# Kernel optimization log

Hardware: AMD Instinct MI355X
Metric: run time of the kernel (lower is better)

## Reference

```python
import jax, jax.numpy as jnp
import numpy as np

POOL = 7
IMG_H, IMG_W = 1024, 1024
EPS = 1e-3  # keras BatchNormalization default epsilon


def crop_and_resize(fmap, boxes, ph, pw):
    # TF tf.image.crop_and_resize (bilinear), box_indices == batch index of each roi.
    # fmap: [B,H,W,C], boxes: [B,N,4] normalized (y1,x1,y2,x2) -> [B,N,ph,pw,C]
    B, H, W, C = fmap.shape
    y1, x1, y2, x2 = jnp.split(boxes, 4, axis=-1)  # each [B,N,1]
    fy = jnp.arange(ph, dtype=boxes.dtype) / (ph - 1)
    fx = jnp.arange(pw, dtype=boxes.dtype) / (pw - 1)
    ys = (y1 + (y2 - y1) * fy) * (H - 1)  # [B,N,ph]
    xs = (x1 + (x2 - x1) * fx) * (W - 1)  # [B,N,pw]
    y0 = jnp.floor(ys)
    x0 = jnp.floor(xs)
    wy = (ys - y0)[:, :, :, None, None]  # [B,N,ph,1,1]
    wx = (xs - x0)[:, :, None, :, None]  # [B,N,1,pw,1]
    y0i = jnp.clip(y0.astype(jnp.int32), 0, H - 1)
    y1i = jnp.clip(y0i + 1, 0, H - 1)
    x0i = jnp.clip(x0.astype(jnp.int32), 0, W - 1)
    x1i = jnp.clip(x0i + 1, 0, W - 1)
    b = jnp.arange(B)[:, None, None, None]
    yi0 = y0i[:, :, :, None]; yi1 = y1i[:, :, :, None]   # [B,N,ph,1]
    xi0 = x0i[:, :, None, :]; xi1 = x1i[:, :, None, :]   # [B,N,1,pw]
    v00 = fmap[b, yi0, xi0]  # [B,N,ph,pw,C]
    v01 = fmap[b, yi0, xi1]
    v10 = fmap[b, yi1, xi0]
    v11 = fmap[b, yi1, xi1]
    top = v00 + (v01 - v00) * wx
    bot = v10 + (v11 - v10) * wx
    return top + (bot - top) * wy


def pyramid_roi_align(rois, fmaps, pool):
    # rois are stop-gradient in the original layer
    rois = jax.lax.stop_gradient(rois)
    y1, x1, y2, x2 = jnp.split(rois, 4, axis=-1)
    h = y2 - y1
    w = x2 - x1
    scale = 256.0 / np.sqrt(float(IMG_H * IMG_W))
    lvl = jnp.log2(jnp.maximum(jnp.sqrt(h * w), 1e-9) / scale)
    lvl = jnp.clip(4 + jnp.round(lvl).astype(jnp.int32), 2, 5)[..., 0]  # [B,N]
    B, N = rois.shape[:2]
    C = fmaps[0].shape[-1]
    out = jnp.zeros((B, N, pool, pool, C), fmaps[0].dtype)
    for i, fm in enumerate(fmaps):  # levels 2..5, fixed small loop
        sel = (lvl == i + 2)[:, :, None, None, None]
        out = jnp.where(sel, crop_and_resize(fm, rois, pool, pool), out)
    return out


def bn_train(x, gamma, beta):
    # keras BatchNorm with training=True: biased batch stats over all axes but channel
    m = x.mean(axis=(0, 1))
    v = x.var(axis=(0, 1))
    return (x - m) * jax.lax.rsqrt(v + EPS) * gamma + beta


def setup_inputs() -> dict:
    key = jax.random.key(0)
    ks = jax.random.split(key, 12)
    B, N, C, F = 2, 1000, 256, 1024
    # rois: valid boxes, sizes spanning all pyramid levels
    tl = jax.random.uniform(ks[0], (B, N, 2), jnp.float32, 0.0, 0.6)
    sz = jax.random.uniform(ks[1], (B, N, 2), jnp.float32, 0.02, 0.4)
    br = jnp.minimum(tl + sz, 1.0)
    rois = jnp.concatenate([tl[..., :1], tl[..., 1:], br[..., :1], br[..., 1:]], axis=-1)
    s = 0.02
    return {
        "rois": rois,
        "p2": jax.random.normal(ks[2], (B, 256, 256, C), jnp.float32),
        "p3": jax.random.normal(ks[3], (B, 128, 128, C), jnp.float32),
        "p4": jax.random.normal(ks[4], (B, 64, 64, C), jnp.float32),
        "p5": jax.random.normal(ks[5], (B, 32, 32, C), jnp.float32),
        "conv1_w": jax.random.normal(ks[6], (POOL, POOL, C, F), jnp.float32) * s,
        "conv1_b": jnp.zeros((F,), jnp.float32),
        "bn1_g": jnp.ones((F,), jnp.float32),
        "bn1_b": jnp.zeros((F,), jnp.float32),
        "conv2_w": jax.random.normal(ks[7], (F, F), jnp.float32) * s,
        "conv2_b": jnp.zeros((F,), jnp.float32),
        "bn2_g": jnp.ones((F,), jnp.float32),
        "bn2_b": jnp.zeros((F,), jnp.float32),
        "cls_w": jax.random.normal(ks[8], (F, 2), jnp.float32) * s,
        "cls_b": jnp.zeros((2,), jnp.float32),
        "delta_w": jax.random.normal(ks[9], (F, 8), jnp.float32) * s,
        "delta_b": jnp.zeros((8,), jnp.float32),
    }


def reference(rois, p2, p3, p4, p5, conv1_w, conv1_b, bn1_g, bn1_b,
              conv2_w, conv2_b, bn2_g, bn2_b, cls_w, cls_b, delta_w, delta_b):
    B, N = rois.shape[:2]
    n_classes = cls_w.shape[-1]
    pooled = pyramid_roi_align(rois, (p2, p3, p4, p5), POOL)  # [B,N,7,7,C]
    # Conv2D(F,(7,7),'valid') on a 7x7 input == full contraction over (h,w,c)
    x = jnp.einsum('bnhwc,hwcf->bnf', pooled, conv1_w) + conv1_b
    x = jax.nn.relu(bn_train(x, bn1_g, bn1_b))
    x = x @ conv2_w + conv2_b  # 1x1 conv == dense
    shared = jax.nn.relu(bn_train(x, bn2_g, bn2_b))  # [B,N,F]
    logits = shared @ cls_w + cls_b                  # [B,N,n_classes]
    probs = jax.nn.softmax(logits, axis=-1)
    deltas = (shared @ delta_w + delta_b).reshape(B, N, n_classes, 4)
    return logits, probs, deltas
```

## Files before the change

### kernel.cpp

```cpp
#include <hip/hip_runtime.h>
#include <hip/hip_bf16.h>

#define NB     2
#define NROI   1000
#define CIN    256
#define FDIM   1024
#define M_ROWS 2000
#define K1     12544
#define EPSBN  1e-3f
#define MN     (M_ROWS * FDIM)

typedef short bf16x8 __attribute__((ext_vector_type(8)));
typedef short bf16x4 __attribute__((ext_vector_type(4)));
typedef float f32x4  __attribute__((ext_vector_type(4)));

__device__ __forceinline__ void gld_lds16(const void* g, void* l) {
  __builtin_amdgcn_global_load_lds((const __attribute__((address_space(1))) char*)g,
                                   (__attribute__((address_space(3))) char*)l, 16, 0, 0);
}

__global__ __launch_bounds__(256) void prep_kernel(
    const float* __restrict__ rois,
    const float* __restrict__ p2, const float* __restrict__ p3,
    const float* __restrict__ p4, const float* __restrict__ p5,
    __hip_bfloat16* __restrict__ pooled,
    const float* __restrict__ conv1_w, __hip_bfloat16* __restrict__ w1t,
    const float* __restrict__ conv2_w, __hip_bfloat16* __restrict__ w2t,
    float* __restrict__ stats) {
  __shared__ float tt[64][65];
  int idx = blockIdx.x;
  int t = threadIdx.x;

  if (idx == 0) {
#pragma unroll
    for (int i = 0; i < 4; i++)
      ((f32x4*)stats)[t + i * 256] = f32x4{0, 0, 0, 0};
    return;
  }

  if (idx < 1 + M_ROWS) {
    int rn = idx - 1;
    int b = rn / NROI;

    const float* roi = rois + (size_t)rn * 4;
    float y1 = roi[0], x1 = roi[1], y2 = roi[2], x2 = roi[3];
    float h = y2 - y1, w = x2 - x1;
    float lvl = log2f(fmaxf(sqrtf(h * w), 1e-9f) * 4.0f);
    int li = 4 + (int)rintf(lvl);
    li = min(max(li, 2), 5) - 2;

    const float* fm; int H;
    switch (li) {
      case 0:  fm = p2; H = 256; break;
      case 1:  fm = p3; H = 128; break;
      case 2:  fm = p4; H = 64;  break;
      default: fm = p5; H = 32;  break;
    }
    int W = H;
    const float* fb = fm + (size_t)b * H * W * CIN;

    int lane = t & 63, wv = t >> 6;
    int c4 = lane * 4;

    for (int pos = wv; pos < 49; pos += 4) {
      int py = pos / 7, px = pos - py * 7;
      float fy = (float)py / 6.0f, fx = (float)px / 6.0f;
      float ys = (y1 + (y2 - y1) * fy) * (float)(H - 1);
      float xs = (x1 + (x2 - x1) * fx) * (float)(W - 1);
      float y0f = floorf(ys), x0f = floorf(xs);
      float wy = ys - y0f, wx = xs - x0f;
      int y0 = min(max((int)y0f, 0), H - 1);
      int x0 = min(max((int)x0f, 0), W - 1);
      int y1i = min(y0 + 1, H - 1);
      int x1i = min(x0 + 1, W - 1);

      f32x4 v00 = *(const f32x4*)(fb + ((size_t)y0 * W + x0) * CIN + c4);
      f32x4 v01 = *(const f32x4*)(fb + ((size_t)y0 * W + x1i) * CIN + c4);
      f32x4 v10 = *(const f32x4*)(fb + ((size_t)y1i * W + x0) * CIN + c4);
      f32x4 v11 = *(const f32x4*)(fb + ((size_t)y1i * W + x1i) * CIN + c4);

      f32x4 top = v00 + (v01 - v00) * wx;
      f32x4 bot = v10 + (v11 - v10) * wx;
      f32x4 val = top + (bot - top) * wy;

      bf16x4 o;
#pragma unroll
      for (int j = 0; j < 4; j++) {
        __hip_bfloat16 hh = __float2bfloat16(val[j]);
        o[j] = *reinterpret_cast<short*>(&hh);
      }
      *(bf16x4*)((short*)pooled + ((size_t)rn * 49 + pos) * CIN + c4) = o;
    }
    return;
  }

  const float* W; short* WT; int K, N, bx, by;
  if (idx < 1 + M_ROWS + 3136) {
    int wk = idx - (1 + M_ROWS);
    W = conv1_w; WT = (short*)w1t; K = K1; N = FDIM;
    bx = wk % 196; by = wk / 196;
  } else {
    int wk = idx - (1 + M_ROWS + 3136);
    W = conv2_w; WT = (short*)w2t; K = FDIM; N = FDIM;
    bx = wk % 16; by = wk / 16;
  }
  int k0 = bx * 64, n0 = by * 64;
  int r = t >> 2, c = t & 3;
#pragma unroll
  for (int i = 0; i < 4; i++) {
    int cg = c * 4 + i;
    f32x4 v = *(const f32x4*)(W + (size_t)(k0 + r) * N + n0 + cg * 4);
#pragma unroll
    for (int j = 0; j < 4; j++) tt[cg * 4 + j][r] = v[j];
  }
  __syncthreads();
  int n = t >> 2, g = t & 3;
#pragma unroll
  for (int i = 0; i < 2; i++) {
    int seg = g * 2 + i;
    bf16x8 o;
#pragma unroll
    for (int j = 0; j < 8; j++) {
      __hip_bfloat16 hh = __float2bfloat16(tt[n][seg * 8 + j]);
      o[j] = *reinterpret_cast<short*>(&hh);
    }
    *(bf16x8*)(WT + (size_t)(n0 + n) * K + k0 + seg * 8) = o;
  }
}

template<int KSLICES>
__global__ __launch_bounds__(512) void gemm8w(const short* __restrict__ A,
                                              const short* __restrict__ BT,
                                              float* __restrict__ P,
                                              int M, int N, int K) {
  __shared__ short As[4 * 128 * 32];
  __shared__ short Bs[4 * 256 * 32];

  int nwg = gridDim.x;
  int bid = blockIdx.x;
  int cpx = nwg >> 3;
  int wg = (bid & 7) * cpx + (bid >> 3);

  int MT = (M + 127) >> 7;
  int NTn = N >> 8;
  int tiles = MT * NTn;
  int ks = wg / tiles;
  int rem = wg % tiles;
  int tm = rem % MT, tn = rem / MT;
  int m0 = tm * 128, n0 = tn * 256;
  int Kc = K / KSLICES;
  int NT = Kc >> 6;
  size_t kb = (size_t)ks * Kc;

  int tid = threadIdx.x;
  int lane = tid & 63, wid = tid >> 6;
  int wr = wid >> 2, wc = wid & 3;

  int srow = tid >> 2;
  int g = (tid & 3) ^ (srow & 3);
  const short* Agb  = A  + (size_t)min(m0 + srow, M - 1) * K + kb + g * 8;
  const short* Bgb0 = BT + (size_t)(n0 + srow) * K + kb + g * 8;
  const short* Bgb1 = Bgb0 + (size_t)128 * K;
  int aoff  = wid * 512;
  int boff0 = wid * 512;
  int boff1 = 4096 + wid * 512;

  int lr = lane & 15;
  int slotoff = ((lane >> 4) ^ (lane & 3)) * 8;
  const short* Ard = As + (wr * 64 + lr) * 32 + slotoff;
  const short* Brd = Bs + (wc * 64 + lr) * 32 + slotoff;

  f32x4 acc[4][4] = {};

#define STAGE(s) do {                                                        \
    int ts_ = (s) >> 1, kh_ = (s) & 1, b_ = ts_ & 1;                         \
    int ko_ = ts_ * 64 + kh_ * 32;                                           \
    short* Ad_ = (short*)As + (b_ * 2 + kh_) * 4096 + aoff;                  \
    short* Bd_ = (short*)Bs + (b_ * 2 + kh_) * 8192;                         \
    gld_lds16(Agb + ko_, Ad_);                                               \
    gld_lds16(Bgb0 + ko_, Bd_ + boff0);                                      \
    gld_lds16(Bgb1 + ko_, Bd_ + boff1);                                      \
  } while (0)

  STAGE(0); STAGE(1); STAGE(2);

  for (int t = 0; t < NT; ++t) {
    int b = t & 1;
#pragma unroll
    for (int kh = 0; kh < 2; ++kh) {
      __builtin_amdgcn_sched_barrier(0);
      if (t < NT - 1)      asm volatile("s_waitcnt vmcnt(6)" ::: "memory");
      else if (kh == 0)    asm volatile("s_waitcnt vmcnt(3)" ::: "memory");
      else                 asm volatile("s_waitcnt vmcnt(0)" ::: "memory");
      __builtin_amdgcn_s_barrier();
      __builtin_amdgcn_sched_barrier(0);

      const short* Ab = Ard + (b * 2 + kh) * 4096;
      const short* Bb = Brd + (b * 2 + kh) * 8192;
      bf16x8 af[4], bf_[4];
#pragma unroll
      for (int mi = 0; mi < 4; mi++) af[mi] = *(const bf16x8*)(Ab + mi * 512);
#pragma unroll
      for (int ni = 0; ni < 4; ni++) bf_[ni] = *(const bf16x8*)(Bb + ni * 512);

      if (kh == 0) { if (t + 1 < NT) STAGE(2 * t + 3); }
      else         { if (t + 2 < NT) STAGE(2 * t + 4); }

      __builtin_amdgcn_sched_barrier(0);
      asm volatile("s_waitcnt lgkmcnt(0)" ::: "memory");
      __builtin_amdgcn_sched_barrier(0);
      __builtin_amdgcn_s_setprio(1);
#pragma unroll
      for (int mi = 0; mi < 4; mi++)
#pragma unroll
        for (int ni = 0; ni < 4; ni++)
          acc[mi][ni] = __builtin_amdgcn_mfma_f32_16x16x32_bf16(af[mi], bf_[ni], acc[mi][ni], 0, 0, 0);
      __builtin_amdgcn_s_setprio(0);
    }
  }
#undef STAGE

  float* Pb = P + (size_t)ks * M * N;
  int crow = (lane >> 4) * 4, ccol = lane & 15;
#pragma unroll
  for (int mi = 0; mi < 4; mi++) {
    int rb = m0 + wr * 64 + mi * 16 + crow;
#pragma unroll
    for (int ni = 0; ni < 4; ni++) {
      int col = n0 + wc * 64 + ni * 16 + ccol;
#pragma unroll
      for (int r = 0; r < 4; r++) {
        int row = rb + r;
        if (row < M) Pb[(size_t)row * N + col] = acc[mi][ni][r];
      }
    }
  }
}

__global__ void reduce_bias_stats(const float* __restrict__ P, const float* __restrict__ bias,
                                  float* __restrict__ X, float* __restrict__ stats,
                                  int M, int KS) {
  int t = threadIdx.x;
  int col = t * 4;
  f32x4 bv = *(const f32x4*)(bias + col);
  f32x4 s = {0, 0, 0, 0}, q = {0, 0, 0, 0};
  for (int r = blockIdx.x; r < M; r += gridDim.x) {
    size_t base = (size_t)r * FDIM + col;
    f32x4 v = *(const f32x4*)(P + base);
    for (int c = 1; c < KS; c++)
      v = v + *(const f32x4*)(P + (size_t)c * MN + base);
    v = v + bv;
    *(f32x4*)(X + base) = v;
    s = s + v;
    q = q + v * v;
  }
#pragma unroll
  for (int j = 0; j < 4; j++) {
    atomicAdd(&stats[col + j], s[j]);
    atomicAdd(&stats[FDIM + col + j], q[j]);
  }
}

__global__ void bn_norm_relu_bf16(const float* __restrict__ X, const float* __restrict__ stats,
                                  const float* __restrict__ g, const float* __restrict__ bta,
                                  __hip_bfloat16* __restrict__ obf, int M) {
  int idx = blockIdx.x * blockDim.x + threadIdx.x;
  if (idx >= M * FDIM) return;
  int f = idx & (FDIM - 1);
  float inv_m = 1.0f / (float)M;
  float mean = stats[f] * inv_m;
  float var = stats[FDIM + f] * inv_m - mean * mean;
  float xn = (X[idx] - mean) * rsqrtf(var + EPSBN) * g[f] + bta[f];
  obf[idx] = __float2bfloat16(fmaxf(xn, 0.0f));
}

__global__ void heads_bn(const float* __restrict__ X2, const float* __restrict__ stats,
                         const float* __restrict__ gg, const float* __restrict__ bb,
                         const float* __restrict__ cls_w, const float* __restrict__ cls_b,
                         const float* __restrict__ dw, const float* __restrict__ db,
                         float* __restrict__ out) {
  int row = blockIdx.x * 4 + (threadIdx.x >> 6);
  int lane = threadIdx.x & 63;
  if (row >= M_ROWS) return;
  const float* xrow = X2 + (size_t)row * FDIM;
  float inv_m = 1.0f / (float)M_ROWS;
  float a[10];
#pragma unroll
  for (int j = 0; j < 10; j++) a[j] = 0.0f;
  for (int k = lane; k < FDIM; k += 64) {
    float mean = stats[k] * inv_m;
    float var = stats[FDIM + k] * inv_m - mean * mean;
    float v = fmaxf((xrow[k] - mean) * rsqrtf(var + EPSBN) * gg[k] + bb[k], 0.0f);
    a[0] += v * cls_w[k * 2 + 0];
    a[1] += v * cls_w[k * 2 + 1];
#pragma unroll
    for (int j = 0; j < 8; j++) a[2 + j] += v * dw[k * 8 + j];
  }
#pragma unroll
  for (int j = 0; j < 10; j++)
    for (int o = 32; o > 0; o >>= 1) a[j] += __shfl_xor(a[j], o, 64);
  if (lane == 0) {
    float l0 = a[0] + cls_b[0], l1 = a[1] + cls_b[1];
    out[row * 2 + 0] = l0;
    out[row * 2 + 1] = l1;
    float mx = fmaxf(l0, l1);
    float e0 = expf(l0 - mx), e1 = expf(l1 - mx);
    float inv = 1.0f / (e0 + e1);
    out[4000 + row * 2 + 0] = e0 * inv;
    out[4000 + row * 2 + 1] = e1 * inv;
#pragma unroll
    for (int j = 0; j < 8; j++) out[8000 + row * 8 + j] = a[2 + j] + db[j];
  }
}

extern "C" void kernel_launch(void* const* d_in, const int* in_sizes, int n_in,
                              void* d_out, int out_size, void* d_ws, size_t ws_size,
                              hipStream_t stream) {
  const float* rois    = (const float*)d_in[0];
  const float* p2      = (const float*)d_in[1];
  const float* p3      = (const float*)d_in[2];
  const float* p4      = (const float*)d_in[3];
  const float* p5      = (const float*)d_in[4];
  const float* conv1_w = (const float*)d_in[5];
  const float* conv1_b = (const float*)d_in[6];
  const float* bn1_g   = (const float*)d_in[7];
  const float* bn1_b   = (const float*)d_in[8];
  const float* conv2_w = (const float*)d_in[9];
  const float* conv2_b = (const float*)d_in[10];
  const float* bn2_g   = (const float*)d_in[11];
  const float* bn2_b   = (const float*)d_in[12];
  const float* cls_w   = (const float*)d_in[13];
  const float* cls_b   = (const float*)d_in[14];
  const float* delta_w = (const float*)d_in[15];
  const float* delta_b = (const float*)d_in[16];
  float* out = (float*)d_out;

  char* ws = (char*)d_ws;
  size_t off = 0;
  __hip_bfloat16* pooled = (__hip_bfloat16*)(ws + off); off += (size_t)M_ROWS * K1 * 2;
  __hip_bfloat16* w1t    = (__hip_bfloat16*)(ws + off); off += (size_t)K1 * FDIM * 2;
  __hip_bfloat16* w2t    = (__hip_bfloat16*)(ws + off); off += (size_t)FDIM * FDIM * 2;
  float* stats1          = (float*)(ws + off);          off += 2 * FDIM * 4;
  float* stats2          = (float*)(ws + off);          off += 2 * FDIM * 4;
  char*  Preg            = ws + off;                    off += (size_t)4 * MN * 4;
  float* part1        = (float*)Preg;
  float* x1           = (float*)Preg;
  __hip_bfloat16* x1n = (__hip_bfloat16*)pooled;
  float* part2        = (float*)Preg;
  float* x2           = (float*)Preg;

  prep_kernel<<<1 + M_ROWS + 3136 + 256, 256, 0, stream>>>(
      rois, p2, p3, p4, p5, pooled, conv1_w, w1t, conv2_w, w2t, stats1);

  gemm8w<4><<<256, 512, 0, stream>>>((const short*)pooled, (const short*)w1t, part1,
                                     M_ROWS, FDIM, K1);
  reduce_bias_stats<<<256, 256, 0, stream>>>(part1, conv1_b, x1, stats1, M_ROWS, 4);

  bn_norm_relu_bf16<<<MN / 256, 256, 0, stream>>>(x1, stats1, bn1_g, bn1_b, x1n, M_ROWS);

  gemm8w<4><<<256, 512, 0, stream>>>((const short*)x1n, (const short*)w2t, part2,
                                     M_ROWS, FDIM, FDIM);
  reduce_bias_stats<<<256, 256, 0, stream>>>(part2, conv2_b, x2, stats2, M_ROWS, 4);

  heads_bn<<<(M_ROWS + 3) / 4, 256, 0, stream>>>(x2, stats2, bn2_g, bn2_b,
                                                 cls_w, cls_b, delta_w, delta_b, out);

  (void)in_sizes; (void)n_in; (void)out_size; (void)ws_size;
}
```

Measured before the change: 210.8 us.

## Deepen GEMM LDS pipeline to six stages, split ROI pooling, restructure heads kernel

The GEMM main loop moves from a double-buffered 2x32 scheme to a six-slot ring of 32-wide K stages with five loads in flight, and K becomes a compile-time template parameter so the loop can be unrolled. The aim is to hide global-to-LDS latency more deeply. ROI pooling now uses two blocks per ROI to give the prep kernel more parallelism. The heads kernel precomputes BN scale/shift and transposed head weights in shared memory and processes 16 rows per block. The deeper ring raises LDS use per block, which may reduce occupancy.

```diff
diff --git a/kernel.cpp b/kernel.cpp
--- a/kernel.cpp
+++ b/kernel.cpp
@@ -18,6 +18,8 @@
   __builtin_amdgcn_global_load_lds((const __attribute__((address_space(1))) char*)g,
                                    (__attribute__((address_space(3))) char*)l, 16, 0, 0);
 }
+
+#define VWAIT(n) asm volatile("s_waitcnt vmcnt(" #n ")" ::: "memory")
 
 __global__ __launch_bounds__(256) void prep_kernel(
     const float* __restrict__ rois,
@@ -38,8 +40,9 @@
     return;
   }
 
-  if (idx < 1 + M_ROWS) {
-    int rn = idx - 1;
+  if (idx < 1 + 2 * M_ROWS) {
+    int rr = idx - 1;
+    int rn = rr >> 1, half = rr & 1;
     int b = rn / NROI;
 
     const float* roi = rois + (size_t)rn * 4;
@@ -62,7 +65,7 @@
     int lane = t & 63, wv = t >> 6;
     int c4 = lane * 4;
 
-    for (int pos = wv; pos < 49; pos += 4) {
+    for (int pos = half * 4 + wv; pos < 49; pos += 8) {
       int py = pos / 7, px = pos - py * 7;
       float fy = (float)py / 6.0f, fx = (float)px / 6.0f;
       float ys = (y1 + (y2 - y1) * fy) * (float)(H - 1);
@@ -95,12 +98,12 @@
   }
 
   const float* W; short* WT; int K, N, bx, by;
-  if (idx < 1 + M_ROWS + 3136) {
-    int wk = idx - (1 + M_ROWS);
+  if (idx < 1 + 2 * M_ROWS + 3136) {
+    int wk = idx - (1 + 2 * M_ROWS);
     W = conv1_w; WT = (short*)w1t; K = K1; N = FDIM;
     bx = wk % 196; by = wk / 196;
   } else {
-    int wk = idx - (1 + M_ROWS + 3136);
+    int wk = idx - (1 + 2 * M_ROWS + 3136);
     W = conv2_w; WT = (short*)w2t; K = FDIM; N = FDIM;
     bx = wk % 16; by = wk / 16;
   }
@@ -128,13 +131,18 @@
   }
 }
 
-template<int KSLICES>
+template<int KSLICES, int KTOT>
 __global__ __launch_bounds__(512) void gemm8w(const short* __restrict__ A,
                                               const short* __restrict__ BT,
                                               float* __restrict__ P,
-                                              int M, int N, int K) {
-  __shared__ short As[4 * 128 * 32];
-  __shared__ short Bs[4 * 256 * 32];
+                                              int M, int N) {
+  constexpr int Kc = KTOT / KSLICES;
+  constexpr int S2 = Kc / 32;
+  static_assert(Kc % 64 == 0 && S2 >= 8, "K slice shape");
+  constexpr int K = KTOT;
+
+  __shared__ short As[6 * 4096];
+  __shared__ short Bs[6 * 8192];
 
   int nwg = gridDim.x;
   int bid = blockIdx.x;
@@ -148,8 +156,6 @@
   int rem = wg % tiles;
   int tm = rem % MT, tn = rem / MT;
   int m0 = tm * 128, n0 = tn * 256;
-  int Kc = K / KSLICES;
-  int NT = Kc >> 6;
   size_t kb = (size_t)ks * Kc;
 
   int tid = threadIdx.x;
@@ -167,58 +173,59 @@
 
   int lr = lane & 15;
   int slotoff = ((lane >> 4) ^ (lane & 3)) * 8;
-  const short* Ard = As + (wr * 64 + lr) * 32 + slotoff;
-  const short* Brd = Bs + (wc * 64 + lr) * 32 + slotoff;
+  const short* Ard  = As + (wr * 64 + lr) * 32 + slotoff;
+  const short* Brd0 = Bs + (wc * 64 + lr) * 32 + slotoff;
+  const short* Brd1 = Brd0 + 3 * 8192;
 
   f32x4 acc[4][4] = {};
 
-#define STAGE(s) do {                                                        \
-    int ts_ = (s) >> 1, kh_ = (s) & 1, b_ = ts_ & 1;                         \
-    int ko_ = ts_ * 64 + kh_ * 32;                                           \
-    short* Ad_ = (short*)As + (b_ * 2 + kh_) * 4096 + aoff;                  \
-    short* Bd_ = (short*)Bs + (b_ * 2 + kh_) * 8192;                         \
-    gld_lds16(Agb + ko_, Ad_);                                               \
-    gld_lds16(Bgb0 + ko_, Bd_ + boff0);                                      \
-    gld_lds16(Bgb1 + ko_, Bd_ + boff1);                                      \
+  auto stage = [&](int s) {
+    int slot = s % 6;
+    int ko = s * 32;
+    short* Ad = (short*)As + slot * 4096 + aoff;
+    short* Bd = (short*)Bs + slot * 8192;
+    gld_lds16(Agb + ko, Ad);
+    gld_lds16(Bgb0 + ko, Bd + boff0);
+    gld_lds16(Bgb1 + ko, Bd + boff1);
+  };
+
+#define PHASE(s_, do_stage)                                                  \
+  do {                                                                       \
+    __builtin_amdgcn_s_barrier();                                            \
+    __builtin_amdgcn_sched_barrier(0);                                       \
+    int slot_ = (s_) % 6;                                                    \
+    const short* Ab_ = Ard + slot_ * 4096;                                   \
+    const short* Bb_ = (slot_ < 3 ? Brd0 : Brd1) + (slot_ % 3) * 8192;       \
+    bf16x8 af_[4], bf_[4];                                                   \
+    _Pragma("unroll")                                                        \
+    for (int mi = 0; mi < 4; mi++) af_[mi] = *(const bf16x8*)(Ab_ + mi * 512);\
+    _Pragma("unroll")                                                        \
+    for (int ni = 0; ni < 4; ni++) bf_[ni] = *(const bf16x8*)(Bb_ + ni * 512);\
+    if (do_stage) stage((s_) + 5);                                           \
+    asm volatile("s_waitcnt lgkmcnt(0)" ::: "memory");                       \
+    __builtin_amdgcn_sched_barrier(0);                                       \
+    __builtin_amdgcn_s_setprio(1);                                           \
+    _Pragma("unroll")                                                        \
+    for (int mi = 0; mi < 4; mi++)                                           \
+      _Pragma("unroll")                                                      \
+      for (int ni = 0; ni < 4; ni++)                                         \
+        acc[mi][ni] = __builtin_amdgcn_mfma_f32_16x16x32_bf16(af_[mi], bf_[ni], acc[mi][ni], 0, 0, 0); \
+    __builtin_amdgcn_s_setprio(0);                                           \
   } while (0)
 
-  STAGE(0); STAGE(1); STAGE(2);
-
-  for (int t = 0; t < NT; ++t) {
-    int b = t & 1;
-#pragma unroll
-    for (int kh = 0; kh < 2; ++kh) {
-      __builtin_amdgcn_sched_barrier(0);
-      if (t < NT - 1)      asm volatile("s_waitcnt vmcnt(6)" ::: "memory");
-      else if (kh == 0)    asm volatile("s_waitcnt vmcnt(3)" ::: "memory");
-      else                 asm volatile("s_waitcnt vmcnt(0)" ::: "memory");
-      __builtin_amdgcn_s_barrier();
-      __builtin_amdgcn_sched_barrier(0);
-
-      const short* Ab = Ard + (b * 2 + kh) * 4096;
-      const short* Bb = Brd + (b * 2 + kh) * 8192;
-      bf16x8 af[4], bf_[4];
-#pragma unroll
-      for (int mi = 0; mi < 4; mi++) af[mi] = *(const bf16x8*)(Ab + mi * 512);
-#pragma unroll
-      for (int ni = 0; ni < 4; ni++) bf_[ni] = *(const bf16x8*)(Bb + ni * 512);
-
-      if (kh == 0) { if (t + 1 < NT) STAGE(2 * t + 3); }
-      else         { if (t + 2 < NT) STAGE(2 * t + 4); }
-
-      __builtin_amdgcn_sched_barrier(0);
-      asm volatile("s_waitcnt lgkmcnt(0)" ::: "memory");
-      __builtin_amdgcn_sched_barrier(0);
-      __builtin_amdgcn_s_setprio(1);
-#pragma unroll
-      for (int mi = 0; mi < 4; mi++)
-#pragma unroll
-        for (int ni = 0; ni < 4; ni++)
-          acc[mi][ni] = __builtin_amdgcn_mfma_f32_16x16x32_bf16(af[mi], bf_[ni], acc[mi][ni], 0, 0, 0);
-      __builtin_amdgcn_s_setprio(0);
-    }
-  }
-#undef STAGE
+  stage(0); stage(1); stage(2); stage(3); stage(4);
+
+#pragma unroll 6
+  for (int s = 0; s < S2 - 5; ++s) {
+    VWAIT(12);
+    PHASE(s, true);
+  }
+  VWAIT(12); PHASE(S2 - 5, false);
+  VWAIT(9);  PHASE(S2 - 4, false);
+  VWAIT(6);  PHASE(S2 - 3, false);
+  VWAIT(3);  PHASE(S2 - 2, false);
+  VWAIT(0);  PHASE(S2 - 1, false);
+#undef PHASE
 
   float* Pb = P + (size_t)ks * M * N;
   int crow = (lane >> 4) * 4, ccol = lane & 15;
@@ -274,42 +281,60 @@
   obf[idx] = __float2bfloat16(fmaxf(xn, 0.0f));
 }
 
-__global__ void heads_bn(const float* __restrict__ X2, const float* __restrict__ stats,
-                         const float* __restrict__ gg, const float* __restrict__ bb,
-                         const float* __restrict__ cls_w, const float* __restrict__ cls_b,
-                         const float* __restrict__ dw, const float* __restrict__ db,
-                         float* __restrict__ out) {
-  int row = blockIdx.x * 4 + (threadIdx.x >> 6);
-  int lane = threadIdx.x & 63;
-  if (row >= M_ROWS) return;
-  const float* xrow = X2 + (size_t)row * FDIM;
+__global__ __launch_bounds__(256) void heads_bn(
+    const float* __restrict__ X2, const float* __restrict__ stats,
+    const float* __restrict__ gg, const float* __restrict__ bb,
+    const float* __restrict__ cls_w, const float* __restrict__ cls_b,
+    const float* __restrict__ dw, const float* __restrict__ db,
+    float* __restrict__ out) {
+  __shared__ float scale[FDIM], shift[FDIM];
+  __shared__ float clsT[2][FDIM];
+  __shared__ float dwT[8][FDIM];
+  int t = threadIdx.x;
   float inv_m = 1.0f / (float)M_ROWS;
-  float a[10];
-#pragma unroll
-  for (int j = 0; j < 10; j++) a[j] = 0.0f;
-  for (int k = lane; k < FDIM; k += 64) {
-    float mean = stats[k] * inv_m;
-    float var = stats[FDIM + k] * inv_m - mean * mean;
-    float v = fmaxf((xrow[k] - mean) * rsqrtf(var + EPSBN) * gg[k] + bb[k], 0.0f);
-    a[0] += v * cls_w[k * 2 + 0];
-    a[1] += v * cls_w[k * 2 + 1];
-#pragma unroll
-    for (int j = 0; j < 8; j++) a[2 + j] += v * dw[k * 8 + j];
-  }
-#pragma unroll
-  for (int j = 0; j < 10; j++)
-    for (int o = 32; o > 0; o >>= 1) a[j] += __shfl_xor(a[j], o, 64);
-  if (lane == 0) {
-    float l0 = a[0] + cls_b[0], l1 = a[1] + cls_b[1];
-    out[row * 2 + 0] = l0;
-    out[row * 2 + 1] = l1;
-    float mx = fmaxf(l0, l1);
-    float e0 = expf(l0 - mx), e1 = expf(l1 - mx);
-    float inv = 1.0f / (e0 + e1);
-    out[4000 + row * 2 + 0] = e0 * inv;
-    out[4000 + row * 2 + 1] = e1 * inv;
-#pragma unroll
-    for (int j = 0; j < 8; j++) out[8000 + row * 8 + j] = a[2 + j] + db[j];
+  for (int i = t; i < FDIM; i += 256) {
+    float m = stats[i] * inv_m;
+    float va = stats[FDIM + i] * inv_m - m * m;
+    float sc = rsqrtf(va + EPSBN) * gg[i];
+    scale[i] = sc;
+    shift[i] = bb[i] - m * sc;
+    clsT[0][i] = cls_w[i * 2];
+    clsT[1][i] = cls_w[i * 2 + 1];
+#pragma unroll
+    for (int j = 0; j < 8; j++) dwT[j][i] = dw[i * 8 + j];
+  }
+  __syncthreads();
+
+  int lane = t & 63, wv = t >> 6;
+#pragma unroll
+  for (int i = 0; i < 4; i++) {
+    int row = blockIdx.x * 16 + i * 4 + wv;
+    const float* xrow = X2 + (size_t)row * FDIM;
+    float a[10];
+#pragma unroll
+    for (int j = 0; j < 10; j++) a[j] = 0.0f;
+    for (int k = lane; k < FDIM; k += 64) {
+      float v = fmaxf(xrow[k] * scale[k] + shift[k], 0.0f);
+      a[0] += v * clsT[0][k];
+      a[1] += v * clsT[1][k];
+#pragma unroll
+      for (int j = 0; j < 8; j++) a[2 + j] += v * dwT[j][k];
+    }
+#pragma unroll
+    for (int j = 0; j < 10; j++)
+      for (int o = 32; o > 0; o >>= 1) a[j] += __shfl_xor(a[j], o, 64);
+    if (lane == 0) {
+      float l0 = a[0] + cls_b[0], l1 = a[1] + cls_b[1];
+      out[row * 2 + 0] = l0;
+      out[row * 2 + 1] = l1;
+      float mx = fmaxf(l0, l1);
+      float e0 = expf(l0 - mx), e1 = expf(l1 - mx);
+      float inv = 1.0f / (e0 + e1);
+      out[4000 + row * 2 + 0] = e0 * inv;
+      out[4000 + row * 2 + 1] = e1 * inv;
+#pragma unroll
+      for (int j = 0; j < 8; j++) out[8000 + row * 8 + j] = a[2 + j] + db[j];
+    }
   }
 }
 
@@ -349,21 +374,21 @@
   float* part2        = (float*)Preg;
   float* x2           = (float*)Preg;
 
-  prep_kernel<<<1 + M_ROWS + 3136 + 256, 256, 0, stream>>>(
+  prep_kernel<<<1 + 2 * M_ROWS + 3136 + 256, 256, 0, stream>>>(
       rois, p2, p3, p4, p5, pooled, conv1_w, w1t, conv2_w, w2t, stats1);
 
-  gemm8w<4><<<256, 512, 0, stream>>>((const short*)pooled, (const short*)w1t, part1,
-                                     M_ROWS, FDIM, K1);
+  gemm8w<4, K1><<<256, 512, 0, stream>>>((const short*)pooled, (const short*)w1t, part1,
+                                         M_ROWS, FDIM);
   reduce_bias_stats<<<256, 256, 0, stream>>>(part1, conv1_b, x1, stats1, M_ROWS, 4);
 
   bn_norm_relu_bf16<<<MN / 256, 256, 0, stream>>>(x1, stats1, bn1_g, bn1_b, x1n, M_ROWS);
 
-  gemm8w<4><<<256, 512, 0, stream>>>((const short*)x1n, (const short*)w2t, part2,
-                                     M_ROWS, FDIM, FDIM);
+  gemm8w<4, FDIM><<<256, 512, 0, stream>>>((const short*)x1n, (const short*)w2t, part2,
+                                           M_ROWS, FDIM);
   reduce_bias_stats<<<256, 256, 0, stream>>>(part2, conv2_b, x2, stats2, M_ROWS, 4);
 
-  heads_bn<<<(M_ROWS + 3) / 4, 256, 0, stream>>>(x2, stats2, bn2_g, bn2_b,
-                                                 cls_w, cls_b, delta_w, delta_b, out);
+  heads_bn<<<125, 256, 0, stream>>>(x2, stats2, bn2_g, bn2_b,
+                                    cls_w, cls_b, delta_w, delta_b, out);
 
   (void)in_sizes; (void)n_in; (void)out_size; (void)ws_size;
 }
```

Result: slower. 228.2 us (+8.3%).

## Replace first GEMM with 128x128 tile kernel using 8 K-slices; vectorize BN

Applied to the files above, without the earlier changes.

Adds a gemm128 kernel with 128x128 tiles, 256 threads and single-buffered LDS, and uses it for the large first GEMM with 8 split-K slices over 1024 workgroups instead of the 256-workgroup gemm8w with 4 slices. This is meant to raise occupancy and spread the big K=12544 contraction across more CUs. In exchange it doubles the partial-sum buffer and the split-K reduction traffic, and loses the double buffering of the old kernel. The BN normalize kernel is also vectorized to process four elements per thread.

```diff
diff --git a/kernel.cpp b/kernel.cpp
--- a/kernel.cpp
+++ b/kernel.cpp
@@ -125,6 +125,89 @@
       o[j] = *reinterpret_cast<short*>(&hh);
     }
     *(bf16x8*)(WT + (size_t)(n0 + n) * K + k0 + seg * 8) = o;
+  }
+}
+
+template<int KSLICES>
+__global__ __launch_bounds__(256) void gemm128(const short* __restrict__ A,
+                                               const short* __restrict__ BT,
+                                               float* __restrict__ P,
+                                               int M, int N, int K) {
+  __shared__ short As[128 * 32];
+  __shared__ short Bs[128 * 32];
+  int nwg = gridDim.x;
+  int bid = blockIdx.x;
+  int cpx = nwg >> 3;
+  int wg = (bid & 7) * cpx + (bid >> 3);
+
+  int MT = (M + 127) >> 7;
+  int NT = N >> 7;
+  int ks   = wg / (MT * NT);
+  int tile = wg % (MT * NT);
+  int tm = tile % MT, tn = tile / MT;
+  int m0 = tm * 128, n0 = tn * 128;
+  int Kc = K / KSLICES;
+  int kb = ks * Kc;
+
+  int t = threadIdx.x;
+  int lane = t & 63, wid = t >> 6;
+  int wr = wid >> 1, wc = wid & 1;
+
+  int q0 = wid * 64 + lane;
+  int q1 = 256 + q0;
+  int as0 = (q0 & 3) * 8, as1 = (q1 & 3) * 8;
+  int ar0 = min(m0 + (q0 >> 2), M - 1);
+  int ar1 = min(m0 + (q1 >> 2), M - 1);
+  const short* Ag0 = A + (size_t)ar0 * K + kb + as0;
+  const short* Ag1 = A + (size_t)ar1 * K + kb + as1;
+  const short* Bg0 = BT + (size_t)(n0 + (q0 >> 2)) * K + kb + as0;
+  const short* Bg1 = BT + (size_t)(n0 + (q1 >> 2)) * K + kb + as1;
+  short* Asb0 = As + wid * 512;
+  short* Asb1 = As + 2048 + wid * 512;
+  short* Bsb0 = Bs + wid * 512;
+  short* Bsb1 = Bs + 2048 + wid * 512;
+
+  int lrow = lane & 15, lk = (lane >> 4) * 8;
+  const short* Ar = As + (wr * 64 + lrow) * 32 + lk;
+  const short* Br = Bs + (wc * 64 + lrow) * 32 + lk;
+
+  f32x4 acc[4][4] = {};
+
+  for (int k0 = 0; k0 < Kc; k0 += 32) {
+    __syncthreads();
+    gld_lds16(Ag0 + k0, Asb0);
+    gld_lds16(Ag1 + k0, Asb1);
+    gld_lds16(Bg0 + k0, Bsb0);
+    gld_lds16(Bg1 + k0, Bsb1);
+    __syncthreads();
+
+    bf16x8 af[4], bfr[4];
+#pragma unroll
+    for (int i = 0; i < 4; i++) {
+      af[i]  = *(const bf16x8*)(Ar + i * 512);
+      bfr[i] = *(const bf16x8*)(Br + i * 512);
+    }
+#pragma unroll
+    for (int mi = 0; mi < 4; mi++)
+#pragma unroll
+      for (int ni = 0; ni < 4; ni++)
+        acc[mi][ni] = __builtin_amdgcn_mfma_f32_16x16x32_bf16(af[mi], bfr[ni], acc[mi][ni], 0, 0, 0);
+  }
+
+  float* Pb = P + (size_t)ks * M * N;
+  int crow = (lane >> 4) * 4, ccol = lane & 15;
+#pragma unroll
+  for (int mi = 0; mi < 4; mi++) {
+    int rb = m0 + wr * 64 + mi * 16 + crow;
+#pragma unroll
+    for (int ni = 0; ni < 4; ni++) {
+      int col = n0 + wc * 64 + ni * 16 + ccol;
+#pragma unroll
+      for (int r = 0; r < 4; r++) {
+        int row = rb + r;
+        if (row < M) Pb[(size_t)row * N + col] = acc[mi][ni][r];
+      }
+    }
   }
 }
 
@@ -264,14 +347,25 @@
 __global__ void bn_norm_relu_bf16(const float* __restrict__ X, const float* __restrict__ stats,
                                   const float* __restrict__ g, const float* __restrict__ bta,
                                   __hip_bfloat16* __restrict__ obf, int M) {
-  int idx = blockIdx.x * blockDim.x + threadIdx.x;
-  if (idx >= M * FDIM) return;
-  int f = idx & (FDIM - 1);
+  int i4 = blockIdx.x * blockDim.x + threadIdx.x;
+  if (i4 * 4 >= M * FDIM) return;
+  int f = (i4 * 4) & (FDIM - 1);
+  f32x4 x  = *(const f32x4*)(X + (size_t)i4 * 4);
+  f32x4 sm = *(const f32x4*)(stats + f);
+  f32x4 sq = *(const f32x4*)(stats + FDIM + f);
+  f32x4 gv = *(const f32x4*)(g + f);
+  f32x4 bv = *(const f32x4*)(bta + f);
   float inv_m = 1.0f / (float)M;
-  float mean = stats[f] * inv_m;
-  float var = stats[FDIM + f] * inv_m - mean * mean;
-  float xn = (X[idx] - mean) * rsqrtf(var + EPSBN) * g[f] + bta[f];
-  obf[idx] = __float2bfloat16(fmaxf(xn, 0.0f));
+  bf16x4 o;
+#pragma unroll
+  for (int j = 0; j < 4; j++) {
+    float mean = sm[j] * inv_m;
+    float var = sq[j] * inv_m - mean * mean;
+    float xn = (x[j] - mean) * rsqrtf(var + EPSBN) * gv[j] + bv[j];
+    __hip_bfloat16 hh = __float2bfloat16(fmaxf(xn, 0.0f));
+    o[j] = *reinterpret_cast<short*>(&hh);
+  }
+  *(bf16x4*)((short*)obf + (size_t)i4 * 4) = o;
 }
 
 __global__ void heads_bn(const float* __restrict__ X2, const float* __restrict__ stats,
@@ -342,7 +436,7 @@
   __hip_bfloat16* w2t    = (__hip_bfloat16*)(ws + off); off += (size_t)FDIM * FDIM * 2;
   float* stats1          = (float*)(ws + off);          off += 2 * FDIM * 4;
   float* stats2          = (float*)(ws + off);          off += 2 * FDIM * 4;
-  char*  Preg            = ws + off;                    off += (size_t)4 * MN * 4;
+  char*  Preg            = ws + off;                    off += (size_t)8 * MN * 4;
   float* part1        = (float*)Preg;
   float* x1           = (float*)Preg;
   __hip_bfloat16* x1n = (__hip_bfloat16*)pooled;
@@ -352,11 +446,11 @@
   prep_kernel<<<1 + M_ROWS + 3136 + 256, 256, 0, stream>>>(
       rois, p2, p3, p4, p5, pooled, conv1_w, w1t, conv2_w, w2t, stats1);
 
-  gemm8w<4><<<256, 512, 0, stream>>>((const short*)pooled, (const short*)w1t, part1,
-                                     M_ROWS, FDIM, K1);
-  reduce_bias_stats<<<256, 256, 0, stream>>>(part1, conv1_b, x1, stats1, M_ROWS, 4);
-
-  bn_norm_relu_bf16<<<MN / 256, 256, 0, stream>>>(x1, stats1, bn1_g, bn1_b, x1n, M_ROWS);
+  gemm128<8><<<1024, 256, 0, stream>>>((const short*)pooled, (const short*)w1t, part1,
+                                       M_ROWS, FDIM, K1);
+  reduce_bias_stats<<<256, 256, 0, stream>>>(part1, conv1_b, x1, stats1, M_ROWS, 8);
+
+  bn_norm_relu_bf16<<<MN / 1024, 256, 0, stream>>>(x1, stats1, bn1_g, bn1_b, x1n, M_ROWS);
 
   gemm8w<4><<<256, 512, 0, stream>>>((const short*)x1n, (const short*)w2t, part2,
                                      M_ROWS, FDIM, FDIM);
```

After: 232.0 us. +10.1%, slower.
